# Kernel tuning notes

Measured on AMD Instinct MI355X. Metric: run time of the kernel, lower is better.

Reference implementation:

```python
import jax, jax.numpy as jnp
import numpy as np

B, L, T = 2048, 4096, 2


def setup_inputs() -> dict:
    key = jax.random.key(0)
    k1, k2, k3, k4, k5 = jax.random.split(key, 5)
    emissions = jax.random.normal(k1, (B, L, T), dtype=jnp.float32)
    # params initialized uniform(-0.1, 0.1) as in the torch module
    transitions = jax.random.uniform(k2, (T, T), minval=-0.1, maxval=0.1, dtype=jnp.float32)
    start_transitions = jax.random.uniform(k3, (T,), minval=-0.1, maxval=0.1, dtype=jnp.float32)
    end_transitions = jax.random.uniform(k4, (T,), minval=-0.1, maxval=0.1, dtype=jnp.float32)
    tags = jax.random.randint(k5, (B, L), 0, T).astype(jnp.int64)
    mask = jnp.ones((B, L), dtype=bool)
    return {"emissions": emissions, "transitions": transitions,
            "start_transitions": start_transitions, "end_transitions": end_transitions,
            "tags": tags, "mask": mask}


def _gold_score(emissions, transitions, start_transitions, end_transitions, tags, mask):
    # score of the given tag path; transitions[to, from]
    score = start_transitions[tags[:, 0]] \
        + jnp.take_along_axis(emissions[:, 0], tags[:, 0:1], axis=1)[:, 0]
    emit = jnp.take_along_axis(emissions[:, 1:], tags[:, 1:, None], axis=2)[..., 0]  # [B, L-1]
    trans = transitions[tags[:, 1:], tags[:, :-1]]                                   # [B, L-1]
    score = score + jnp.sum((emit + trans) * mask[:, 1:].astype(emit.dtype), axis=1)
    last_idx = jnp.sum(mask, axis=1).astype(jnp.int32) - 1
    last_tags = jnp.take_along_axis(tags, last_idx[:, None].astype(tags.dtype), axis=1)[:, 0]
    return score + end_transitions[last_tags]


def _normalizer(emissions, transitions, start_transitions, end_transitions, mask):
    # forward algorithm in log space via lax.scan over time
    alpha0 = start_transitions + emissions[:, 0]  # [B, T]

    def step(alpha, inp):
        emit, m = inp  # emit: [B, T], m: [B]
        scores = alpha[:, None, :] + transitions[None, :, :]  # [B, to, from]
        alpha_new = jax.nn.logsumexp(scores, axis=2) + emit
        alpha = jnp.where(m[:, None], alpha_new, alpha)
        return alpha, None

    emit_t = jnp.swapaxes(emissions[:, 1:], 0, 1)  # [L-1, B, T]
    mask_t = jnp.swapaxes(mask[:, 1:], 0, 1)       # [L-1, B]
    alpha, _ = jax.lax.scan(step, alpha0, (emit_t, mask_t))
    return jax.nn.logsumexp(alpha + end_transitions, axis=1)


def reference(emissions, transitions, start_transitions, end_transitions, tags, mask):
    """CRF NLL loss (reduction='mean'), per-token normalized, as in CRFLayer._compute_loss."""
    gold = _gold_score(emissions, transitions, start_transitions, end_transitions, tags, mask)
    logZ = _normalizer(emissions, transitions, start_transitions, end_transitions, mask)
    seq_lengths = jnp.clip(jnp.sum(mask, axis=1).astype(emissions.dtype), 1.0)
    nll = (logZ - gold) / seq_lengths
    return jnp.mean(nll)
```

## Files before the change

### kernel.cpp

```cpp
#include <hip/hip_runtime.h>
#include <math.h>

#define LSEQ  4096
#define BATCH 2048
#define CHUNK 16
#define BLOCK 256
#define LOG2E 1.4426950408889634f
#define LN2   0.6931471805599453f

__device__ __forceinline__ float exp2_fast(float x) {
    float r; asm("v_exp_f32 %0, %1" : "=v"(r) : "v"(x)); return r;
}
__device__ __forceinline__ float log2_fast(float x) {
    float r; asm("v_log_f32 %0, %1" : "=v"(r) : "v"(x)); return r;
}
__device__ __forceinline__ float lse2b(float a, float b) {
    float m = fmaxf(a, b);
    float d = fminf(a, b) - m;
    return m + log2_fast(1.0f + exp2_fast(d));
}

__global__ __launch_bounds__(BLOCK) void crf_row_kernel(
    const float* __restrict__ emis,
    const float* __restrict__ trans,
    const float* __restrict__ startt,
    const float* __restrict__ endt,
    const int*   __restrict__ tags,
    float*       __restrict__ nll_out)
{
    const int b    = blockIdx.x;
    const int tid  = threadIdx.x;
    const int lane = tid & 63;
    const int wave = tid >> 6;
    const int t0   = tid * CHUNK;

    const float t00 = trans[0], t01 = trans[1], t10 = trans[2], t11 = trans[3];
    const float T00 = t00 * LOG2E, T01 = t01 * LOG2E, T10 = t10 * LOG2E, T11 = t11 * LOG2E;
    const float s0 = startt[0], s1 = startt[1];

    const float4* erow = reinterpret_cast<const float4*>(emis + ((size_t)b * LSEQ + t0) * 2);
    float e0[CHUNK], e1[CHUNK];
    #pragma unroll
    for (int i = 0; i < 8; ++i) {
        float4 v = erow[i];
        e0[2*i]   = v.x; e1[2*i]   = v.y;
        e0[2*i+1] = v.z; e1[2*i+1] = v.w;
    }

    const int4* trow = reinterpret_cast<const int4*>(tags + (size_t)b * LSEQ + t0);
    int tg[CHUNK];
    #pragma unroll
    for (int i = 0; i < 4; ++i) {
        int4 v = trow[i];
        tg[4*i] = v.x; tg[4*i+1] = v.y; tg[4*i+2] = v.z; tg[4*i+3] = v.w;
    }
    const int pidx = (tid == 0) ? 0 : (t0 - 1);
    const int prev = tags[(size_t)b * LSEQ + pidx];

    float g = 0.0f;
    int c11, ccur, cprev; float Pf;
    if (tid == 0) {
        g = tg[0] ? s1 : s0;
        c11 = 0; ccur = 0; cprev = 0; Pf = 15.0f;
    } else {
        c11 = tg[0] & prev; ccur = tg[0]; cprev = prev; Pf = 16.0f;
    }
    g += tg[0] ? e1[0] : e0[0];
    int p = tg[0];
    #pragma unroll
    for (int i = 1; i < CHUNK; ++i) {
        g    += tg[i] ? e1[i] : e0[i];
        c11  += tg[i] & p;
        ccur += tg[i];
        cprev += p;
        p = tg[i];
    }
    if (tid == BLOCK - 1) g += tg[CHUNK-1] ? endt[1] : endt[0];
    {
        float f11 = (float)c11, fc = (float)ccur, fp = (float)cprev;
        g += t11 * f11 + t10 * (fc - f11) + t01 * (fp - f11)
           + t00 * (Pf - fc - fp + f11);
    }

    float A00, A01, A10, A11, B00, B01, B10, B11;
    if (tid == 0) {
        float v0 = (s0 + e0[0]) * LOG2E;
        float v1 = (s1 + e1[0]) * LOG2E;
        A00 = v0; A01 = v0; A10 = v1; A11 = v1;
    } else {
        float f0 = e0[0] * LOG2E, f1 = e1[0] * LOG2E;
        A00 = T00 + f0; A01 = T01 + f0; A10 = T10 + f1; A11 = T11 + f1;
    }
    {
        float f0 = e0[8] * LOG2E, f1 = e1[8] * LOG2E;
        B00 = T00 + f0; B01 = T01 + f0; B10 = T10 + f1; B11 = T11 + f1;
    }
    #pragma unroll
    for (int i = 1; i < 8; ++i) {
        float fa0 = e0[i] * LOG2E,   fa1 = e1[i] * LOG2E;
        float fb0 = e0[i+8] * LOG2E, fb1 = e1[i+8] * LOG2E;
        float nA00 = lse2b(T00 + A00, T01 + A10) + fa0;
        float nA01 = lse2b(T00 + A01, T01 + A11) + fa0;
        float nA10 = lse2b(T10 + A00, T11 + A10) + fa1;
        float nA11 = lse2b(T10 + A01, T11 + A11) + fa1;
        float nB00 = lse2b(T00 + B00, T01 + B10) + fb0;
        float nB01 = lse2b(T00 + B01, T01 + B11) + fb0;
        float nB10 = lse2b(T10 + B00, T11 + B10) + fb1;
        float nB11 = lse2b(T10 + B01, T11 + B11) + fb1;
        A00 = nA00; A01 = nA01; A10 = nA10; A11 = nA11;
        B00 = nB00; B01 = nB01; B10 = nB10; B11 = nB11;
    }
    float M00 = lse2b(B00 + A00, B01 + A10);
    float M01 = lse2b(B00 + A01, B01 + A11);
    float M10 = lse2b(B10 + A00, B11 + A10);
    float M11 = lse2b(B10 + A01, B11 + A11);

    #pragma unroll
    for (int s = 1; s < 64; s <<= 1) {
        float p00 = __shfl_down(M00, s, 64);
        float p01 = __shfl_down(M01, s, 64);
        float p10 = __shfl_down(M10, s, 64);
        float p11 = __shfl_down(M11, s, 64);
        float pg  = __shfl_down(g,   s, 64);
        float n00 = lse2b(p00 + M00, p01 + M10);
        float n01 = lse2b(p00 + M01, p01 + M11);
        float n10 = lse2b(p10 + M00, p11 + M10);
        float n11 = lse2b(p10 + M01, p11 + M11);
        M00 = n00; M01 = n01; M10 = n10; M11 = n11;
        g += pg;
    }

    __shared__ float sM[4][4];
    __shared__ float sg[4];
    if (lane == 0) {
        sM[wave][0] = M00; sM[wave][1] = M01; sM[wave][2] = M10; sM[wave][3] = M11;
        sg[wave] = g;
    }
    __syncthreads();
    if (tid == 0) {
        float a00 = sM[0][0], a01 = sM[0][1], a10 = sM[0][2], a11 = sM[0][3];
        float b00 = sM[1][0], b01 = sM[1][1], b10 = sM[1][2], b11 = sM[1][3];
        float c00 = sM[2][0], c01 = sM[2][1], c10 = sM[2][2], c11f = sM[2][3];
        float d00 = sM[3][0], d01 = sM[3][1], d10 = sM[3][2], d11 = sM[3][3];
        float X00 = lse2b(b00 + a00, b01 + a10);
        float X10 = lse2b(b10 + a00, b11 + a10);
        float Y00 = lse2b(d00 + c00, d01 + c10);
        float Y01 = lse2b(d00 + c01, d01 + c11f);
        float Y10 = lse2b(d10 + c00, d11 + c10);
        float Y11 = lse2b(d10 + c01, d11 + c11f);
        float Z00 = lse2b(Y00 + X00, Y01 + X10);
        float Z10 = lse2b(Y10 + X00, Y11 + X10);
        float logZ = lse2b(Z00 + endt[0] * LOG2E, Z10 + endt[1] * LOG2E) * LN2;
        float gall = (sg[0] + sg[1]) + (sg[2] + sg[3]);
        nll_out[b] = (logZ - gall) * (1.0f / (float)LSEQ);
    }
}

__global__ __launch_bounds__(256) void mean_kernel(
    const float* __restrict__ nll, float* __restrict__ out)
{
    int tid = threadIdx.x;
    const float4* v = reinterpret_cast<const float4*>(nll);
    float4 a = v[tid], b = v[tid + 256];
    float acc = ((a.x + a.y) + (a.z + a.w)) + ((b.x + b.y) + (b.z + b.w));
    #pragma unroll
    for (int s = 1; s < 64; s <<= 1) acc += __shfl_down(acc, s, 64);
    __shared__ float sw[4];
    if ((tid & 63) == 0) sw[tid >> 6] = acc;
    __syncthreads();
    if (tid == 0) out[0] = ((sw[0] + sw[1]) + (sw[2] + sw[3])) * (1.0f / (float)BATCH);
}

extern "C" void kernel_launch(void* const* d_in, const int* in_sizes, int n_in,
                              void* d_out, int out_size, void* d_ws, size_t ws_size,
                              hipStream_t stream) {
    const float* emis   = (const float*)d_in[0];
    const float* trans  = (const float*)d_in[1];
    const float* startt = (const float*)d_in[2];
    const float* endt   = (const float*)d_in[3];
    const int*   tags   = (const int*)d_in[4];

    float* nll = (float*)d_ws;
    float* out = (float*)d_out;

    crf_row_kernel<<<BATCH, BLOCK, 0, stream>>>(emis, trans, startt, endt, tags, nll);
    mean_kernel<<<1, 256, 0, stream>>>(nll, out);
}
```

Measured before the change: 27.46 us.

## Run per-chunk CRF recurrence in linear probability space with rank-one chunk summaries

Replaces the log-space 2x2 matrix recurrence inside each thread's chunk with a linear-space product, using exponentiated transitions and emissions so each step needs multiplies and FMAs instead of exp/log pairs. Each chunk's transfer matrix is then compressed into a rank-one form (two log column sums plus a ratio beta), which shrinks the wave shuffle tree and the cross-wave combine from four values to three. This cuts transcendental count and shuffle traffic. It risks overflow or underflow over a 16-step chunk with large emissions, and it relies on the chunk matrix being effectively rank-one, which only holds for the 2-tag positive transition structure.

```diff
diff --git a/kernel.cpp b/kernel.cpp
--- a/kernel.cpp
+++ b/kernel.cpp
@@ -35,8 +35,9 @@
     const int t0   = tid * CHUNK;
 
     const float t00 = trans[0], t01 = trans[1], t10 = trans[2], t11 = trans[3];
-    const float T00 = t00 * LOG2E, T01 = t01 * LOG2E, T10 = t10 * LOG2E, T11 = t11 * LOG2E;
     const float s0 = startt[0], s1 = startt[1];
+    const float P00 = exp2_fast(t00 * LOG2E), P01 = exp2_fast(t01 * LOG2E);
+    const float P10 = exp2_fast(t10 * LOG2E), P11 = exp2_fast(t11 * LOG2E);
 
     const float4* erow = reinterpret_cast<const float4*>(emis + ((size_t)b * LSEQ + t0) * 2);
     float e0[CHUNK], e1[CHUNK];
@@ -82,77 +83,62 @@
            + t00 * (Pf - fc - fp + f11);
     }
 
-    float A00, A01, A10, A11, B00, B01, B10, B11;
-    if (tid == 0) {
-        float v0 = (s0 + e0[0]) * LOG2E;
-        float v1 = (s1 + e1[0]) * LOG2E;
-        A00 = v0; A01 = v0; A10 = v1; A11 = v1;
-    } else {
-        float f0 = e0[0] * LOG2E, f1 = e1[0] * LOG2E;
-        A00 = T00 + f0; A01 = T01 + f0; A10 = T10 + f1; A11 = T11 + f1;
-    }
+    float a0, a1, b0c, b1c;
     {
-        float f0 = e0[8] * LOG2E, f1 = e1[8] * LOG2E;
-        B00 = T00 + f0; B01 = T01 + f0; B10 = T10 + f1; B11 = T11 + f1;
+        float E0 = exp2_fast(e0[0] * LOG2E);
+        float E1 = exp2_fast(e1[0] * LOG2E);
+        if (tid == 0) {
+            a0 = exp2_fast((s0 + e0[0]) * LOG2E);
+            a1 = exp2_fast((s1 + e1[0]) * LOG2E);
+            b0c = a0; b1c = a1;
+        } else {
+            a0  = P00 * E0; a1  = P10 * E1;
+            b0c = P01 * E0; b1c = P11 * E1;
+        }
     }
     #pragma unroll
-    for (int i = 1; i < 8; ++i) {
-        float fa0 = e0[i] * LOG2E,   fa1 = e1[i] * LOG2E;
-        float fb0 = e0[i+8] * LOG2E, fb1 = e1[i+8] * LOG2E;
-        float nA00 = lse2b(T00 + A00, T01 + A10) + fa0;
-        float nA01 = lse2b(T00 + A01, T01 + A11) + fa0;
-        float nA10 = lse2b(T10 + A00, T11 + A10) + fa1;
-        float nA11 = lse2b(T10 + A01, T11 + A11) + fa1;
-        float nB00 = lse2b(T00 + B00, T01 + B10) + fb0;
-        float nB01 = lse2b(T00 + B01, T01 + B11) + fb0;
-        float nB10 = lse2b(T10 + B00, T11 + B10) + fb1;
-        float nB11 = lse2b(T10 + B01, T11 + B11) + fb1;
-        A00 = nA00; A01 = nA01; A10 = nA10; A11 = nA11;
-        B00 = nB00; B01 = nB01; B10 = nB10; B11 = nB11;
+    for (int i = 1; i < CHUNK; ++i) {
+        float F0 = exp2_fast(e0[i] * LOG2E);
+        float F1 = exp2_fast(e1[i] * LOG2E);
+        float na0 = F0 * fmaf(P00, a0,  P01 * a1);
+        float na1 = F1 * fmaf(P10, a0,  P11 * a1);
+        float nb0 = F0 * fmaf(P00, b0c, P01 * b1c);
+        float nb1 = F1 * fmaf(P10, b0c, P11 * b1c);
+        a0 = na0; a1 = na1; b0c = nb0; b1c = nb1;
     }
-    float M00 = lse2b(B00 + A00, B01 + A10);
-    float M01 = lse2b(B00 + A01, B01 + A11);
-    float M10 = lse2b(B10 + A00, B11 + A10);
-    float M11 = lse2b(B10 + A01, B11 + A11);
+
+    float lc0  = log2_fast(a0);
+    float lc1  = log2_fast(a1);
+    float beta = log2_fast(b0c) - lc0;
 
     #pragma unroll
     for (int s = 1; s < 64; s <<= 1) {
-        float p00 = __shfl_down(M00, s, 64);
-        float p01 = __shfl_down(M01, s, 64);
-        float p10 = __shfl_down(M10, s, 64);
-        float p11 = __shfl_down(M11, s, 64);
-        float pg  = __shfl_down(g,   s, 64);
-        float n00 = lse2b(p00 + M00, p01 + M10);
-        float n01 = lse2b(p00 + M01, p01 + M11);
-        float n10 = lse2b(p10 + M00, p11 + M10);
-        float n11 = lse2b(p10 + M01, p11 + M11);
-        M00 = n00; M01 = n01; M10 = n10; M11 = n11;
-        g += pg;
+        float plc0 = __shfl_down(lc0,  s, 64);
+        float plc1 = __shfl_down(lc1,  s, 64);
+        float pb   = __shfl_down(beta, s, 64);
+        float pg   = __shfl_down(g,    s, 64);
+        float sv = lse2b(lc0, lc1 + pb);
+        lc0 = plc0 + sv;
+        lc1 = plc1 + sv;
+        g  += pg;
     }
 
-    __shared__ float sM[4][4];
-    __shared__ float sg[4];
+    __shared__ float sR[4][4];
     if (lane == 0) {
-        sM[wave][0] = M00; sM[wave][1] = M01; sM[wave][2] = M10; sM[wave][3] = M11;
-        sg[wave] = g;
+        sR[wave][0] = lc0; sR[wave][1] = lc1; sR[wave][2] = beta; sR[wave][3] = g;
     }
     __syncthreads();
     if (tid == 0) {
-        float a00 = sM[0][0], a01 = sM[0][1], a10 = sM[0][2], a11 = sM[0][3];
-        float b00 = sM[1][0], b01 = sM[1][1], b10 = sM[1][2], b11 = sM[1][3];
-        float c00 = sM[2][0], c01 = sM[2][1], c10 = sM[2][2], c11f = sM[2][3];
-        float d00 = sM[3][0], d01 = sM[3][1], d10 = sM[3][2], d11 = sM[3][3];
-        float X00 = lse2b(b00 + a00, b01 + a10);
-        float X10 = lse2b(b10 + a00, b11 + a10);
-        float Y00 = lse2b(d00 + c00, d01 + c10);
-        float Y01 = lse2b(d00 + c01, d01 + c11f);
-        float Y10 = lse2b(d10 + c00, d11 + c10);
-        float Y11 = lse2b(d10 + c01, d11 + c11f);
-        float Z00 = lse2b(Y00 + X00, Y01 + X10);
-        float Z10 = lse2b(Y10 + X00, Y11 + X10);
-        float logZ = lse2b(Z00 + endt[0] * LOG2E, Z10 + endt[1] * LOG2E) * LN2;
-        float gall = (sg[0] + sg[1]) + (sg[2] + sg[3]);
-        nll_out[b] = (logZ - gall) * (1.0f / (float)LSEQ);
+        float c0 = sR[0][0], c1 = sR[0][1], gg = sR[0][3];
+        #pragma unroll
+        for (int w = 1; w < 4; ++w) {
+            float sv = lse2b(c0, c1 + sR[w][2]);
+            c0 = sR[w][0] + sv;
+            c1 = sR[w][1] + sv;
+            gg += sR[w][3];
+        }
+        float logZ = lse2b(c0 + endt[0] * LOG2E, c1 + endt[1] * LOG2E) * LN2;
+        nll_out[b] = (logZ - gg) * (1.0f / (float)LSEQ);
     }
 }
 
```

Result: faster. 23.81 us (-13.3%).
